# Kernel tuning notes

Hardware: AMD Instinct MI355X
Metric: run time of the kernel (lower is better)

Reference implementation:

```python
import jax, jax.numpy as jnp
import numpy as np

NUM_CLASSES = 10
MARGIN = 1.0


def setup_inputs() -> dict:
    key = jax.random.key(0)
    k1, k2 = jax.random.split(key)
    N, D = 8192, 128
    embeddings = jax.random.normal(k1, (N, D), dtype=jnp.float32)
    labels = jax.random.randint(k2, (N,), 0, NUM_CLASSES)
    return {"embeddings": embeddings, "labels": labels}


def _batch_hard_loss(embeddings, labels):
    # embeddings: [N, D] float, labels: [N] int in [0, NUM_CLASSES)
    N = embeddings.shape[0]
    x2 = jnp.sum(embeddings * embeddings, axis=1)  # [N]
    # squared euclidean pairwise distances via gram trick, clamped at 0
    d = jnp.maximum(x2[:, None] + x2[None, :] - 2.0 * (embeddings @ embeddings.T), 0.0)  # [N, N]
    same = labels[:, None] == labels[None, :]  # [N, N]

    # hardest positive: max squared distance over same-class (includes self, as in source)
    d_pos = jnp.max(jnp.where(same, d, -jnp.inf), axis=1)  # [N]

    # FAITHFUL TO SOURCE BUG: negative_distances[k] = sum_{j: label_j != k} d(i, j)
    # = T_i - S_i(k), where S_i(k) = sum over class-k members of d(i, j)
    onehot = jax.nn.one_hot(labels, NUM_CLASSES, dtype=d.dtype)  # [N, 10]
    S = d @ onehot  # [N, 10]
    T = jnp.sum(d, axis=1)  # [N]
    neg_dist = T[:, None] - S  # [N, 10]
    k_star = jnp.argmin(neg_dist, axis=1)  # [N], values in [0, 10)

    # negatives list for class c is ordered by (class, then index); take the k_star-th element
    order = jnp.argsort(labels * N + jnp.arange(N))  # global (class, index) order
    mask_sorted = (~same)[:, order]  # [N, N] negatives of anchor i, in list order
    cs = jnp.cumsum(mask_sorted.astype(jnp.int32), axis=1)
    cond = mask_sorted & (cs == (k_star[:, None] + 1))
    pos_in_sorted = jnp.argmax(cond, axis=1)  # first position with rank k_star
    j_star = order[pos_in_sorted]  # [N] index of the "worst negative"
    d_neg = d[jnp.arange(N), j_star]  # [N]

    # base TripletLoss: relu(d_pos - d_neg + margin); mean over batch (use_gt_than_zero_mean=False)
    loss = jax.nn.relu(d_pos - d_neg + MARGIN)
    return jnp.mean(loss)


def reference(embeddings, labels):
    return _batch_hard_loss(embeddings, labels)
```

## Files before the change

### kernel.cpp

```cpp
#include <hip/hip_runtime.h>
#include <hip/hip_bf16.h>

#define BH_N 8192
#define BH_D 128
#define BH_NC 10
#define BH_MARGIN 1.0f
#define NSEG 4
#define MAXTILES (BH_N / 32 + BH_NC)

typedef __attribute__((ext_vector_type(8)))  short bf16x8;
typedef __attribute__((ext_vector_type(16))) float f32x16;

#define OFF_R(r) (((r) & 3) + 8 * ((r) >> 2))

__device__ __forceinline__ unsigned short f2bf(float f) {
    unsigned u = __float_as_uint(f);
    u += 0x7fffu + ((u >> 16) & 1u);
    return (unsigned short)(u >> 16);
}

__global__ __launch_bounds__(1024) void bh_sort(const int* __restrict__ labels,
                                                int* __restrict__ perm,
                                                int* __restrict__ labs,
                                                int* __restrict__ cstart,
                                                int* __restrict__ zreg,
                                                float* __restrict__ out) {
    const int t = threadIdx.x;
    for (int i = t; i < BH_NC * BH_D + 16 + BH_N; i += 1024) zreg[i] = 0;
    if (t == 0) out[0] = 0.0f;

    const int lane = t & 63, w = t >> 6;
    const int4* lp = (const int4*)labels;
    const int4 a = lp[t * 2], b = lp[t * 2 + 1];
    int L[8] = {a.x, a.y, a.z, a.w, b.x, b.y, b.z, b.w};

    int lh[BH_NC];
#pragma unroll
    for (int c = 0; c < BH_NC; c++) lh[c] = 0;
#pragma unroll
    for (int k = 0; k < 8; k++) {
#pragma unroll
        for (int c = 0; c < BH_NC; c++) lh[c] += (L[k] == c);
    }
    int inc[BH_NC];
#pragma unroll
    for (int c = 0; c < BH_NC; c++) inc[c] = lh[c];
    for (int m = 1; m < 64; m <<= 1) {
#pragma unroll
        for (int c = 0; c < BH_NC; c++) {
            const int o = __shfl_up(inc[c], m);
            if (lane >= m) inc[c] += o;
        }
    }
    __shared__ int wtot[16][BH_NC];
    __shared__ int cst[BH_NC + 1];
    if (lane == 63) {
#pragma unroll
        for (int c = 0; c < BH_NC; c++) wtot[w][c] = inc[c];
    }
    __syncthreads();
    if (t == 0) {
        int run = 0;
#pragma unroll
        for (int c = 0; c < BH_NC; c++) {
            int tot = 0;
            for (int w2 = 0; w2 < 16; w2++) tot += wtot[w2][c];
            cst[c] = run; run += tot;
        }
        cst[BH_NC] = run;
#pragma unroll
        for (int c = 0; c <= BH_NC; c++) cstart[c] = cst[c];
    }
    __syncthreads();
    int wpre[BH_NC];
#pragma unroll
    for (int c = 0; c < BH_NC; c++) {
        int s = cst[c];
        for (int w2 = 0; w2 < w; w2++) s += wtot[w2][c];
        wpre[c] = s + inc[c] - lh[c];
    }
#pragma unroll
    for (int k = 0; k < 8; k++) {
        const int j = t * 8 + k;
        const int Lk = L[k];
        int pos = 0;
#pragma unroll
        for (int c = 0; c < BH_NC; c++) pos += (Lk == c) ? wpre[c] : 0;
        perm[pos] = j;
        labs[pos] = Lk;
#pragma unroll
        for (int c = 0; c < BH_NC; c++) wpre[c] += (Lk == c);
    }
}

__global__ __launch_bounds__(256) void bh_permute(const float* __restrict__ E,
                                                  const int* __restrict__ perm,
                                                  const int* __restrict__ labs,
                                                  unsigned short* __restrict__ Es,
                                                  float* __restrict__ x2s,
                                                  float* __restrict__ M,
                                                  float* __restrict__ sumx2) {
    __shared__ float vbuf[8][132];
    __shared__ float x2r[8];
    __shared__ int lab8[8];
    const int t = threadIdx.x;
    const int r = t >> 5, sub = t & 31;
    const int row = blockIdx.x * 8 + r;
    const int oi = perm[row];
    const float4 v = ((const float4*)(E + (size_t)oi * BH_D))[sub];
    ushort4 h;
    h.x = f2bf(v.x); h.y = f2bf(v.y); h.z = f2bf(v.z); h.w = f2bf(v.w);
    ((ushort4*)(Es + (size_t)row * BH_D))[sub] = h;
    *(float4*)(&vbuf[r][sub * 4]) = v;
    float s = v.x * v.x + v.y * v.y + v.z * v.z + v.w * v.w;
#pragma unroll
    for (int m = 1; m < 32; m <<= 1) s += __shfl_xor(s, m);
    if (sub == 0) { x2s[row] = s; x2r[r] = s; lab8[r] = labs[row]; }
    __syncthreads();
    if (t < BH_D) {
        int c = lab8[0]; float acc = 0.0f;
#pragma unroll
        for (int rr = 0; rr < 8; rr++) {
            const int cr = lab8[rr];
            if (cr != c) { atomicAdd(&M[(size_t)c * BH_D + t], acc); acc = 0.0f; c = cr; }
            acc += vbuf[rr][t];
        }
        atomicAdd(&M[(size_t)c * BH_D + t], acc);
    } else if (t == BH_D) {
        int c = lab8[0]; float a2 = 0.0f;
#pragma unroll
        for (int rr = 0; rr < 8; rr++) {
            const int cr = lab8[rr];
            if (cr != c) { atomicAdd(&sumx2[c], a2); a2 = 0.0f; c = cr; }
            a2 += x2r[rr];
        }
        atomicAdd(&sumx2[c], a2);
    }
}

__global__ __launch_bounds__(64) void bh_dpos(const unsigned short* __restrict__ Es,
                                              const float* __restrict__ x2s,
                                              const int* __restrict__ cstart,
                                              int* __restrict__ dposU) {
    const int tile = blockIdx.x / NSEG;
    const int seg  = blockIdx.x % NSEG;
    int cs[BH_NC + 1];
#pragma unroll
    for (int c = 0; c <= BH_NC; c++) cs[c] = cstart[c];
    int c = -1, t0 = 0, base = 0;
#pragma unroll
    for (int cc = 0; cc < BH_NC; cc++) {
        const int len = cs[cc + 1] - cs[cc];
        const int nt = (len + 31) >> 5;
        if (c < 0 && tile < base + nt) { c = cc; t0 = tile - base; }
        base += nt;
    }
    if (c < 0) return;
    const int c0 = cs[c], c1 = cs[c + 1], len = c1 - c0;
    const int rb = c0 + t0 * 32;
    const int nch = (len + 31) >> 5;
    const int per = (nch + NSEG - 1) / NSEG;
    const int jb0 = c0 + seg * per * 32;
    if (jb0 >= c1) return;
    const int jb1 = min(jb0 + per * 32, c1);

    const int lane = threadIdx.x;
    const int cid = lane & 31, half = lane >> 5;
    const int rowbase = rb + 4 * half;

    bf16x8 afrag[8];
    {
        const int ar = min(rb + cid, BH_N - 1);
        const unsigned short* arow = Es + (size_t)ar * BH_D + half * 8;
#pragma unroll
        for (int ks = 0; ks < 8; ks++) afrag[ks] = *(const bf16x8*)(arow + ks * 16);
    }
    float xr[16];
#pragma unroll
    for (int r = 0; r < 16; r++) xr[r] = x2s[min(rowbase + OFF_R(r), BH_N - 1)];

    float dpos[16];
#pragma unroll
    for (int r = 0; r < 16; r++) dpos[r] = 0.0f;

    int jcl = min(jb0 + cid, c1 - 1);
    bf16x8 bcur[8];
    {
        const unsigned short* brow = Es + (size_t)jcl * BH_D + half * 8;
#pragma unroll
        for (int ks = 0; ks < 8; ks++) bcur[ks] = *(const bf16x8*)(brow + ks * 16);
    }
    float xc = x2s[jcl];

    for (int jb = jb0; jb < jb1; jb += 32) {
        const int jcln = min(jb + 32 + cid, c1 - 1);
        bf16x8 bnxt[8];
        {
            const unsigned short* brow = Es + (size_t)jcln * BH_D + half * 8;
#pragma unroll
            for (int ks = 0; ks < 8; ks++) bnxt[ks] = *(const bf16x8*)(brow + ks * 16);
        }
        const float xcn = x2s[jcln];

        f32x16 acc = {0.0f, 0.0f, 0.0f, 0.0f, 0.0f, 0.0f, 0.0f, 0.0f,
                      0.0f, 0.0f, 0.0f, 0.0f, 0.0f, 0.0f, 0.0f, 0.0f};
#pragma unroll
        for (int ks = 0; ks < 8; ks++)
            acc = __builtin_amdgcn_mfma_f32_32x32x16_bf16(afrag[ks], bcur[ks], acc, 0, 0, 0);

        const bool vm = (jb + cid) < jb1;
#pragma unroll
        for (int r = 0; r < 16; r++) {
            const float dd = fmaxf(fmaf(-2.0f, acc[r], xr[r] + xc), 0.0f);
            const bool rowin = (rowbase + OFF_R(r)) < c1;
            dpos[r] = fmaxf(dpos[r], (vm && rowin) ? dd : 0.0f);
        }
#pragma unroll
        for (int ks = 0; ks < 8; ks++) bcur[ks] = bnxt[ks];
        xc = xcn;
    }
#pragma unroll
    for (int r = 0; r < 16; r++) {
#pragma unroll
        for (int m = 1; m < 32; m <<= 1) dpos[r] = fmaxf(dpos[r], __shfl_xor(dpos[r], m));
    }
    if (cid == 0) {
#pragma unroll
        for (int r = 0; r < 16; r++) {
            const int row = rowbase + OFF_R(r);
            if (row < c1) atomicMax(&dposU[row], __float_as_int(dpos[r]));
        }
    }
}

__global__ __launch_bounds__(256) void bh_select(const float* __restrict__ E,
                                                 const float* __restrict__ x2s,
                                                 const int* __restrict__ labs,
                                                 const int* __restrict__ cstart,
                                                 const int* __restrict__ perm,
                                                 const float* __restrict__ M,
                                                 const float* __restrict__ sumx2,
                                                 const int* __restrict__ dposU,
                                                 float* __restrict__ out) {
    const int w = threadIdx.x >> 6, lane = threadIdx.x & 63;
    const int spos = blockIdx.x * 4 + w;
    const int oi = perm[spos];
    const float2 u0 = ((const float2*)(E + (size_t)oi * BH_D))[lane];

    float dc[BH_NC];
#pragma unroll
    for (int c = 0; c < BH_NC; c++) {
        const float2 mv = ((const float2*)(M + (size_t)c * BH_D))[lane];
        dc[c] = u0.x * mv.x + u0.y * mv.y;
    }
#pragma unroll
    for (int m = 1; m < 64; m <<= 1) {
#pragma unroll
        for (int c = 0; c < BH_NC; c++) dc[c] += __shfl_xor(dc[c], m);
    }
    const float x2i = x2s[spos];
    int cs0[BH_NC + 1];
#pragma unroll
    for (int c = 0; c <= BH_NC; c++) cs0[c] = cstart[c];

    float T = 0.0f, Sk[BH_NC];
#pragma unroll
    for (int c = 0; c < BH_NC; c++) {
        const float cnt = (float)(cs0[c + 1] - cs0[c]);
        Sk[c] = cnt * x2i + sumx2[c] - 2.0f * dc[c];
        T += Sk[c];
    }
    int kstar = 0; float best = T - Sk[0];
#pragma unroll
    for (int c = 1; c < BH_NC; c++) {
        const float nd = T - Sk[c];
        if (nd < best) { best = nd; kstar = c; }
    }

    const int a  = labs[spos];
    const int sa = cs0[a], ea = cs0[a + 1];
    const int p  = (kstar < sa) ? kstar : (ea + (kstar - sa));
    const int oj = perm[p];

    const float2 u1 = ((const float2*)(E + (size_t)oj * BH_D))[lane];
    float dp = u0.x * u1.x + u0.y * u1.y;
#pragma unroll
    for (int m = 1; m < 64; m <<= 1) dp += __shfl_xor(dp, m);
    const float dneg = fmaxf(x2i + x2s[p] - 2.0f * dp, 0.0f);

    const float dposv = __int_as_float(dposU[spos]);
    const float loss = fmaxf(dposv - dneg + BH_MARGIN, 0.0f);

    __shared__ float ls[4];
    if (lane == 0) ls[w] = loss;
    __syncthreads();
    if (threadIdx.x == 0)
        atomicAdd(out, (ls[0] + ls[1] + ls[2] + ls[3]) * (1.0f / (float)BH_N));
}

extern "C" void kernel_launch(void* const* d_in, const int* in_sizes, int n_in,
                              void* d_out, int out_size, void* d_ws, size_t ws_size,
                              hipStream_t stream) {
    const float* E = (const float*)d_in[0];
    const int* labels = (const int*)d_in[1];
    float* out = (float*)d_out;

    unsigned short* Es = (unsigned short*)d_ws;
    float* x2s   = (float*)(Es + (size_t)BH_N * BH_D);
    float* M     = x2s + BH_N;
    float* sumx2 = M + BH_NC * BH_D;
    int*   dposU = (int*)(sumx2 + 16);
    int*   perm  = dposU + BH_N;
    int*   labs  = perm + BH_N;
    int*   cstart= labs + BH_N;

    bh_sort<<<1, 1024, 0, stream>>>(labels, perm, labs, cstart, (int*)M, out);
    bh_permute<<<BH_N / 8, 256, 0, stream>>>(E, perm, labs, Es, x2s, M, sumx2);
    bh_dpos<<<MAXTILES * NSEG, 64, 0, stream>>>(Es, x2s, cstart, dposU);
    bh_select<<<BH_N / 4, 256, 0, stream>>>(E, x2s, labs, cstart, perm, M, sumx2, dposU, out);
}
```

Baseline: 128.1 us.

## Restructure select to one thread per row on bf16 data, tweak sort and permute

The select kernel changes from one wavefront per anchor on fp32 embeddings to one thread per anchor reading the sorted bf16 copy. This removes the perm/labs indirection and the cross-lane shuffle reductions, and derives the class from cstart. The loss is reduced per wavefront before one atomic. Separately, the sort kernel parallelises the per-class wave prefix, and permute handles 16 rows per 512-thread block. The bf16 dot products change numerics for d_neg and the class distances, a dead duplicate dp loop is left in, and per-thread row reads are strided and uncoalesced.

New measurement: 106.1 us. 1.21x faster.

```diff
diff --git a/kernel.cpp b/kernel.cpp
--- a/kernel.cpp
+++ b/kernel.cpp
@@ -17,6 +17,9 @@
     unsigned u = __float_as_uint(f);
     u += 0x7fffu + ((u >> 16) & 1u);
     return (unsigned short)(u >> 16);
+}
+__device__ __forceinline__ float bf2f(short h) {
+    return __uint_as_float(((unsigned)(unsigned short)h) << 16);
 }
 
 __global__ __launch_bounds__(1024) void bh_sort(const int* __restrict__ labels,
@@ -45,6 +48,7 @@
     int inc[BH_NC];
 #pragma unroll
     for (int c = 0; c < BH_NC; c++) inc[c] = lh[c];
+#pragma unroll
     for (int m = 1; m < 64; m <<= 1) {
 #pragma unroll
         for (int c = 0; c < BH_NC; c++) {
@@ -53,20 +57,25 @@
         }
     }
     __shared__ int wtot[16][BH_NC];
+    __shared__ int wpref[16][BH_NC];
+    __shared__ int ctot[BH_NC];
     __shared__ int cst[BH_NC + 1];
     if (lane == 63) {
 #pragma unroll
         for (int c = 0; c < BH_NC; c++) wtot[w][c] = inc[c];
+    }
+    __syncthreads();
+    if (t < BH_NC) {
+        int run = 0;
+#pragma unroll
+        for (int w2 = 0; w2 < 16; w2++) { wpref[w2][t] = run; run += wtot[w2][t]; }
+        ctot[t] = run;
     }
     __syncthreads();
     if (t == 0) {
         int run = 0;
 #pragma unroll
-        for (int c = 0; c < BH_NC; c++) {
-            int tot = 0;
-            for (int w2 = 0; w2 < 16; w2++) tot += wtot[w2][c];
-            cst[c] = run; run += tot;
-        }
+        for (int c = 0; c < BH_NC; c++) { cst[c] = run; run += ctot[c]; }
         cst[BH_NC] = run;
 #pragma unroll
         for (int c = 0; c <= BH_NC; c++) cstart[c] = cst[c];
@@ -74,11 +83,7 @@
     __syncthreads();
     int wpre[BH_NC];
 #pragma unroll
-    for (int c = 0; c < BH_NC; c++) {
-        int s = cst[c];
-        for (int w2 = 0; w2 < w; w2++) s += wtot[w2][c];
-        wpre[c] = s + inc[c] - lh[c];
-    }
+    for (int c = 0; c < BH_NC; c++) wpre[c] = cst[c] + wpref[w][c] + inc[c] - lh[c];
 #pragma unroll
     for (int k = 0; k < 8; k++) {
         const int j = t * 8 + k;
@@ -93,19 +98,19 @@
     }
 }
 
-__global__ __launch_bounds__(256) void bh_permute(const float* __restrict__ E,
+__global__ __launch_bounds__(512) void bh_permute(const float* __restrict__ E,
                                                   const int* __restrict__ perm,
                                                   const int* __restrict__ labs,
                                                   unsigned short* __restrict__ Es,
                                                   float* __restrict__ x2s,
                                                   float* __restrict__ M,
                                                   float* __restrict__ sumx2) {
-    __shared__ float vbuf[8][132];
-    __shared__ float x2r[8];
-    __shared__ int lab8[8];
+    __shared__ float vbuf[16][132];
+    __shared__ float x2r[16];
+    __shared__ int lab16[16];
     const int t = threadIdx.x;
     const int r = t >> 5, sub = t & 31;
-    const int row = blockIdx.x * 8 + r;
+    const int row = blockIdx.x * 16 + r;
     const int oi = perm[row];
     const float4 v = ((const float4*)(E + (size_t)oi * BH_D))[sub];
     ushort4 h;
@@ -115,22 +120,22 @@
     float s = v.x * v.x + v.y * v.y + v.z * v.z + v.w * v.w;
 #pragma unroll
     for (int m = 1; m < 32; m <<= 1) s += __shfl_xor(s, m);
-    if (sub == 0) { x2s[row] = s; x2r[r] = s; lab8[r] = labs[row]; }
+    if (sub == 0) { x2s[row] = s; x2r[r] = s; lab16[r] = labs[row]; }
     __syncthreads();
     if (t < BH_D) {
-        int c = lab8[0]; float acc = 0.0f;
-#pragma unroll
-        for (int rr = 0; rr < 8; rr++) {
-            const int cr = lab8[rr];
+        int c = lab16[0]; float acc = 0.0f;
+#pragma unroll
+        for (int rr = 0; rr < 16; rr++) {
+            const int cr = lab16[rr];
             if (cr != c) { atomicAdd(&M[(size_t)c * BH_D + t], acc); acc = 0.0f; c = cr; }
             acc += vbuf[rr][t];
         }
         atomicAdd(&M[(size_t)c * BH_D + t], acc);
     } else if (t == BH_D) {
-        int c = lab8[0]; float a2 = 0.0f;
-#pragma unroll
-        for (int rr = 0; rr < 8; rr++) {
-            const int cr = lab8[rr];
+        int c = lab16[0]; float a2 = 0.0f;
+#pragma unroll
+        for (int rr = 0; rr < 16; rr++) {
+            const int cr = lab16[rr];
             if (cr != c) { atomicAdd(&sumx2[c], a2); a2 = 0.0f; c = cr; }
             a2 += x2r[rr];
         }
@@ -233,41 +238,47 @@
     }
 }
 
-__global__ __launch_bounds__(256) void bh_select(const float* __restrict__ E,
-                                                 const float* __restrict__ x2s,
-                                                 const int* __restrict__ labs,
-                                                 const int* __restrict__ cstart,
-                                                 const int* __restrict__ perm,
-                                                 const float* __restrict__ M,
-                                                 const float* __restrict__ sumx2,
-                                                 const int* __restrict__ dposU,
-                                                 float* __restrict__ out) {
-    const int w = threadIdx.x >> 6, lane = threadIdx.x & 63;
-    const int spos = blockIdx.x * 4 + w;
-    const int oi = perm[spos];
-    const float2 u0 = ((const float2*)(E + (size_t)oi * BH_D))[lane];
+__global__ __launch_bounds__(64) void bh_select(const unsigned short* __restrict__ Es,
+                                                const float* __restrict__ x2s,
+                                                const int* __restrict__ cstart,
+                                                const float* __restrict__ M,
+                                                const float* __restrict__ sumx2,
+                                                const int* __restrict__ dposU,
+                                                float* __restrict__ out) {
+    const int lane = threadIdx.x;
+    const int spos = blockIdx.x * 64 + lane;
+
+    int cs[BH_NC + 1];
+#pragma unroll
+    for (int c = 0; c <= BH_NC; c++) cs[c] = cstart[c];
+
+    bf16x8 u0[16];
+    const unsigned short* rp = Es + (size_t)spos * BH_D;
+#pragma unroll
+    for (int k = 0; k < 16; k++) u0[k] = *(const bf16x8*)(rp + k * 8);
 
     float dc[BH_NC];
 #pragma unroll
+    for (int c = 0; c < BH_NC; c++) dc[c] = 0.0f;
+#pragma unroll
+    for (int k = 0; k < 16; k++) {
+        float ef[8];
+#pragma unroll
+        for (int d = 0; d < 8; d++) ef[d] = bf2f(u0[k][d]);
+#pragma unroll
+        for (int c = 0; c < BH_NC; c++) {
+            const float4 m0 = *(const float4*)(M + (size_t)c * BH_D + k * 8);
+            const float4 m1 = *(const float4*)(M + (size_t)c * BH_D + k * 8 + 4);
+            dc[c] += ef[0] * m0.x + ef[1] * m0.y + ef[2] * m0.z + ef[3] * m0.w
+                   + ef[4] * m1.x + ef[5] * m1.y + ef[6] * m1.z + ef[7] * m1.w;
+        }
+    }
+
+    const float x2i = x2s[spos];
+    float T = 0.0f, Sk[BH_NC];
+#pragma unroll
     for (int c = 0; c < BH_NC; c++) {
-        const float2 mv = ((const float2*)(M + (size_t)c * BH_D))[lane];
-        dc[c] = u0.x * mv.x + u0.y * mv.y;
-    }
-#pragma unroll
-    for (int m = 1; m < 64; m <<= 1) {
-#pragma unroll
-        for (int c = 0; c < BH_NC; c++) dc[c] += __shfl_xor(dc[c], m);
-    }
-    const float x2i = x2s[spos];
-    int cs0[BH_NC + 1];
-#pragma unroll
-    for (int c = 0; c <= BH_NC; c++) cs0[c] = cstart[c];
-
-    float T = 0.0f, Sk[BH_NC];
-#pragma unroll
-    for (int c = 0; c < BH_NC; c++) {
-        const float cnt = (float)(cs0[c + 1] - cs0[c]);
-        Sk[c] = cnt * x2i + sumx2[c] - 2.0f * dc[c];
+        Sk[c] = (float)(cs[c + 1] - cs[c]) * x2i + sumx2[c] - 2.0f * dc[c];
         T += Sk[c];
     }
     int kstar = 0; float best = T - Sk[0];
@@ -277,25 +288,33 @@
         if (nd < best) { best = nd; kstar = c; }
     }
 
-    const int a  = labs[spos];
-    const int sa = cs0[a], ea = cs0[a + 1];
-    const int p  = (kstar < sa) ? kstar : (ea + (kstar - sa));
-    const int oj = perm[p];
-
-    const float2 u1 = ((const float2*)(E + (size_t)oj * BH_D))[lane];
-    float dp = u0.x * u1.x + u0.y * u1.y;
-#pragma unroll
-    for (int m = 1; m < 64; m <<= 1) dp += __shfl_xor(dp, m);
+    int a = 0;
+#pragma unroll
+    for (int c = 1; c < BH_NC; c++) a += (spos >= cs[c]);
+    const int p = (kstar < cs[a]) ? kstar : (cs[a + 1] + (kstar - cs[a]));
+
+    const unsigned short* qp = Es + (size_t)p * BH_D;
+    float dp = 0.0f;
+#pragma unroll
+    for (int k = 0; k < 16; k++) {
+        const bf16x8 u1 = *(const bf16x8*)(qp + k * 8);
+#pragma unroll
+        for (int d = 0; d < 8; d++) dp += bf2f(u0[k][d]) * bf2f(u1[d == 0 ? 0 : d]);
+    }
+    dp = 0.0f;
+#pragma unroll
+    for (int k = 0; k < 16; k++) {
+        const bf16x8 u1 = *(const bf16x8*)(qp + k * 8);
+#pragma unroll
+        for (int d = 0; d < 8; d++) dp = fmaf(bf2f(u0[k][d]), bf2f(u1[d]), dp);
+    }
     const float dneg = fmaxf(x2i + x2s[p] - 2.0f * dp, 0.0f);
 
     const float dposv = __int_as_float(dposU[spos]);
-    const float loss = fmaxf(dposv - dneg + BH_MARGIN, 0.0f);
-
-    __shared__ float ls[4];
-    if (lane == 0) ls[w] = loss;
-    __syncthreads();
-    if (threadIdx.x == 0)
-        atomicAdd(out, (ls[0] + ls[1] + ls[2] + ls[3]) * (1.0f / (float)BH_N));
+    float loss = fmaxf(dposv - dneg + BH_MARGIN, 0.0f);
+#pragma unroll
+    for (int m = 1; m < 64; m <<= 1) loss += __shfl_xor(loss, m);
+    if (lane == 0) atomicAdd(out, loss * (1.0f / (float)BH_N));
 }
 
 extern "C" void kernel_launch(void* const* d_in, const int* in_sizes, int n_in,
@@ -315,7 +334,7 @@
     int*   cstart= labs + BH_N;
 
     bh_sort<<<1, 1024, 0, stream>>>(labels, perm, labs, cstart, (int*)M, out);
-    bh_permute<<<BH_N / 8, 256, 0, stream>>>(E, perm, labs, Es, x2s, M, sumx2);
+    bh_permute<<<BH_N / 16, 512, 0, stream>>>(E, perm, labs, Es, x2s, M, sumx2);
     bh_dpos<<<MAXTILES * NSEG, 64, 0, stream>>>(Es, x2s, cstart, dposU);
-    bh_select<<<BH_N / 4, 256, 0, stream>>>(E, x2s, labs, cstart, perm, M, sumx2, dposU, out);
-}
+    bh_select<<<BH_N / 64, 64, 0, stream>>>(Es, x2s, cstart, M, sumx2, dposU, out);
+}
```
